# Kernel optimization log

Measured on AMD Instinct MI355X. Metric: run time of the kernel, lower is better.

Reference implementation:

```python
import jax, jax.numpy as jnp
import numpy as np

EPS = 1e-5          # calc_mean_std eps
C = 256             # feature channels
N_PER = 32          # patches per side-group
SIDES = (24, 32, 48)
OUT = 56            # AdaptiveAvgPool2d target


def _pool_matrix(s, o=OUT):
    """Exact torch AdaptiveAvgPool2d as a [o, s] averaging matrix."""
    P = np.zeros((o, s), np.float32)
    for i in range(o):
        start = (i * s) // o
        end = -((-(i + 1) * s) // o)  # ceil((i+1)*s/o)
        P[i, start:end] = 1.0 / (end - start)
    return jnp.asarray(P)

_POOL = {s: _pool_matrix(s) for s in SIDES}


def setup_inputs() -> dict:
    key = jax.random.key(0)
    ks = jax.random.split(key, len(SIDES))
    out = {}
    means, stds = [], []
    for k, s in zip(ks, SIDES):
        raw = jax.random.normal(k, (N_PER, C, s, s), dtype=jnp.float32)
        # calc_mean_std: per (patch, channel) spatial mean / unbiased std
        m = raw.mean(axis=(2, 3), keepdims=True)
        v = raw.var(axis=(2, 3), keepdims=True, ddof=1)
        sd = jnp.sqrt(v + EPS)
        out[f"patches_{s}"] = (raw - m) / sd  # pre-normalized, as in __init__
        means.append(m)
        stds.append(sd)
    out["style_mean"] = jnp.concatenate(means, axis=0)  # [96, C, 1, 1]
    out["style_std"] = jnp.concatenate(stds, axis=0)    # [96, C, 1, 1]
    return out


def _denorm_relu_pool(x, mean, std, P):
    # x: [n, C, s, s]; affine denorm + ReLU + adaptive avg pool to 56x56
    t = jax.nn.relu(x * std + mean)
    y = jnp.einsum('oi,ncij->ncoj', P, t)   # pool rows
    y = jnp.einsum('ncoj,pj->ncop', y, P)   # pool cols
    return y


def reference(patches_24, patches_32, patches_48, style_mean, style_std):
    groups = ((patches_24, 24, 0), (patches_32, 32, N_PER), (patches_48, 48, 2 * N_PER))
    outs = []
    for x, s, lo in groups:
        n = x.shape[0]
        outs.append(_denorm_relu_pool(x, style_mean[lo:lo + n], style_std[lo:lo + n], _POOL[s]))
    return jnp.concatenate(outs, axis=0)  # [96, C, 56, 56]
```

## Files before the change

### kernel.cpp

```cpp
#include <hip/hip_runtime.h>


#define C_CH 256
#define OUTS 56
#define NPER 32

template<int S>
__device__ __forceinline__ void group_body(const float* __restrict__ x,
                                           const float* __restrict__ smean,
                                           const float* __restrict__ sstd,
                                           float* __restrict__ out,
                                           int local_bid, int n_base,
                                           float* __restrict__ lds) {
    const int n_local = local_bid >> 8;
    const int c       = local_bid & 255;
    const int n_glob  = n_base + n_local;
    const float mn = smean[n_glob * C_CH + c];
    const float sd = sstd [n_glob * C_CH + c];

    const float* xin = x + (size_t)(n_local * C_CH + c) * (S * S);
    const int tid = threadIdx.x;

    constexpr int NV = (S * S) / 4;
    const float4* x4 = (const float4*)xin;
    float4* l4 = (float4*)lds;
    for (int idx = tid; idx < NV; idx += 256) {
        float4 v = x4[idx];
        v.x = fmaxf(fmaf(v.x, sd, mn), 0.0f);
        v.y = fmaxf(fmaf(v.y, sd, mn), 0.0f);
        v.z = fmaxf(fmaf(v.z, sd, mn), 0.0f);
        v.w = fmaxf(fmaf(v.w, sd, mn), 0.0f);
        l4[idx] = v;
    }
    __syncthreads();

    float* outp = out + (size_t)(n_glob * C_CH + c) * (OUTS * OUTS);
    float4* out4 = (float4*)outp;

    constexpr int NQ = (OUTS * OUTS) / 4;
    for (int q = tid; q < NQ; q += 256) {
        const int i  = q / (OUTS / 4);
        const int j0 = (q % (OUTS / 4)) * 4;
        const int r0 = (i * S) / OUTS;
        const int r1 = ((i + 1) * S + OUTS - 1) / OUTS;
        const int rc = r1 - r0;

        float o[4];
        #pragma unroll
        for (int k = 0; k < 4; ++k) {
            const int j  = j0 + k;
            const int c0 = (j * S) / OUTS;
            const int c1 = ((j + 1) * S + OUTS - 1) / OUTS;
            const int cc = c1 - c0;
            float acc = lds[r0 * S + c0];
            if (cc == 2) acc += lds[r0 * S + c0 + 1];
            if (rc == 2) {
                acc += lds[(r0 + 1) * S + c0];
                if (cc == 2) acc += lds[(r0 + 1) * S + c0 + 1];
            }
            o[k] = acc * (1.0f / (float)(rc * cc));
        }
        float4 v; v.x = o[0]; v.y = o[1]; v.z = o[2]; v.w = o[3];
        out4[q] = v;
    }
}

__global__ __launch_bounds__(256) void PPIN_DC_20753281974843_kernel(
        const float* __restrict__ p24, const float* __restrict__ p32,
        const float* __restrict__ p48, const float* __restrict__ smean,
        const float* __restrict__ sstd, float* __restrict__ out) {
    __shared__ float lds[48 * 48];
    const int bid   = blockIdx.x;
    const int group = bid >> 13;
    const int local = bid & 8191;
    if (group == 0)      group_body<24>(p24, smean, sstd, out, local, 0,        lds);
    else if (group == 1) group_body<32>(p32, smean, sstd, out, local, NPER,     lds);
    else                 group_body<48>(p48, smean, sstd, out, local, 2 * NPER, lds);
}

extern "C" void kernel_launch(void* const* d_in, const int* in_sizes, int n_in,
                              void* d_out, int out_size, void* d_ws, size_t ws_size,
                              hipStream_t stream) {
    const float* p24   = (const float*)d_in[0];
    const float* p32   = (const float*)d_in[1];
    const float* p48   = (const float*)d_in[2];
    const float* smean = (const float*)d_in[3];
    const float* sstd  = (const float*)d_in[4];
    float* out = (float*)d_out;

    PPIN_DC_20753281974843_kernel<<<dim3(24576), dim3(256), 0, stream>>>(
        p24, p32, p48, smean, sstd, out);
}
```

Measured before the change: 391.4 us.

## Process two channels per block with interleaved LDS and branchless 2x2 pooling

Measured after the change: 401.0 us. 2.4% more time.

```diff
diff --git a/kernel.cpp b/kernel.cpp
--- a/kernel.cpp
+++ b/kernel.cpp
@@ -11,57 +11,71 @@
                                            const float* __restrict__ sstd,
                                            float* __restrict__ out,
                                            int local_bid, int n_base,
-                                           float* __restrict__ lds) {
-    const int n_local = local_bid >> 8;
-    const int c       = local_bid & 255;
+                                           float2* __restrict__ lds2) {
+    const int n_local = local_bid >> 7;
+    const int pair    = local_bid & 127;
+    const int ch      = pair * 2;
     const int n_glob  = n_base + n_local;
-    const float mn = smean[n_glob * C_CH + c];
-    const float sd = sstd [n_glob * C_CH + c];
 
-    const float* xin = x + (size_t)(n_local * C_CH + c) * (S * S);
+    const float2 mn = *(const float2*)(smean + n_glob * C_CH + ch);
+    const float2 sd = *(const float2*)(sstd  + n_glob * C_CH + ch);
+
+    const float* xa = x + (size_t)(n_local * C_CH + ch) * (S * S);
+    const float4* a4 = (const float4*)xa;
+    const float4* b4 = (const float4*)(xa + S * S);
+    float4* l4 = (float4*)lds2;
+
     const int tid = threadIdx.x;
 
     constexpr int NV = (S * S) / 4;
-    const float4* x4 = (const float4*)xin;
-    float4* l4 = (float4*)lds;
     for (int idx = tid; idx < NV; idx += 256) {
-        float4 v = x4[idx];
-        v.x = fmaxf(fmaf(v.x, sd, mn), 0.0f);
-        v.y = fmaxf(fmaf(v.y, sd, mn), 0.0f);
-        v.z = fmaxf(fmaf(v.z, sd, mn), 0.0f);
-        v.w = fmaxf(fmaf(v.w, sd, mn), 0.0f);
-        l4[idx] = v;
+        float4 va = a4[idx];
+        float4 vb = b4[idx];
+        va.x = fmaxf(fmaf(va.x, sd.x, mn.x), 0.0f);
+        va.y = fmaxf(fmaf(va.y, sd.x, mn.x), 0.0f);
+        va.z = fmaxf(fmaf(va.z, sd.x, mn.x), 0.0f);
+        va.w = fmaxf(fmaf(va.w, sd.x, mn.x), 0.0f);
+        vb.x = fmaxf(fmaf(vb.x, sd.y, mn.y), 0.0f);
+        vb.y = fmaxf(fmaf(vb.y, sd.y, mn.y), 0.0f);
+        vb.z = fmaxf(fmaf(vb.z, sd.y, mn.y), 0.0f);
+        vb.w = fmaxf(fmaf(vb.w, sd.y, mn.y), 0.0f);
+        float4 lo; lo.x = va.x; lo.y = vb.x; lo.z = va.y; lo.w = vb.y;
+        float4 hi; hi.x = va.z; hi.y = vb.z; hi.z = va.w; hi.w = vb.w;
+        l4[2 * idx]     = lo;
+        l4[2 * idx + 1] = hi;
     }
     __syncthreads();
 
-    float* outp = out + (size_t)(n_glob * C_CH + c) * (OUTS * OUTS);
-    float4* out4 = (float4*)outp;
+    float* outA = out + (size_t)(n_glob * C_CH + ch) * (OUTS * OUTS);
+    float4* oa4 = (float4*)outA;
+    float4* ob4 = (float4*)(outA + OUTS * OUTS);
 
     constexpr int NQ = (OUTS * OUTS) / 4;
     for (int q = tid; q < NQ; q += 256) {
         const int i  = q / (OUTS / 4);
-        const int j0 = (q % (OUTS / 4)) * 4;
-        const int r0 = (i * S) / OUTS;
-        const int r1 = ((i + 1) * S + OUTS - 1) / OUTS;
-        const int rc = r1 - r0;
+        const int j0 = (q - i * (OUTS / 4)) * 4;
+        const int rA = (i * S) / OUTS;
+        const int rB = ((i + 1) * S - 1) / OUTS;
+        const float2* rowA = lds2 + rA * S;
+        const float2* rowB = lds2 + rB * S;
 
-        float o[4];
+        float oA[4], oB[4];
         #pragma unroll
         for (int k = 0; k < 4; ++k) {
             const int j  = j0 + k;
-            const int c0 = (j * S) / OUTS;
-            const int c1 = ((j + 1) * S + OUTS - 1) / OUTS;
-            const int cc = c1 - c0;
-            float acc = lds[r0 * S + c0];
-            if (cc == 2) acc += lds[r0 * S + c0 + 1];
-            if (rc == 2) {
-                acc += lds[(r0 + 1) * S + c0];
-                if (cc == 2) acc += lds[(r0 + 1) * S + c0 + 1];
-            }
-            o[k] = acc * (1.0f / (float)(rc * cc));
+            const int cA = (j * S) / OUTS;
+            const int cB = ((j + 1) * S - 1) / OUTS;
+            const float2 v0 = rowA[cA];
+            const float2 v1 = rowA[cB];
+            const float2 v2 = rowB[cA];
+            const float2 v3 = rowB[cB];
+            oA[k] = 0.25f * ((v0.x + v1.x) + (v2.x + v3.x));
+            oB[k] = 0.25f * ((v0.y + v1.y) + (v2.y + v3.y));
         }
-        float4 v; v.x = o[0]; v.y = o[1]; v.z = o[2]; v.w = o[3];
-        out4[q] = v;
+        float4 sa; sa.x = oA[0]; sa.y = oA[1]; sa.z = oA[2]; sa.w = oA[3];
+        float4 sb; sb.x = oB[0]; sb.y = oB[1]; sb.z = oB[2]; sb.w = oB[3];
+        oa4[q] = sa;
+        ob4[q] = sb;
     }
 }
 
@@ -69,13 +83,13 @@
         const float* __restrict__ p24, const float* __restrict__ p32,
         const float* __restrict__ p48, const float* __restrict__ smean,
         const float* __restrict__ sstd, float* __restrict__ out) {
-    __shared__ float lds[48 * 48];
+    __shared__ float2 lds2[48 * 48];
     const int bid   = blockIdx.x;
-    const int group = bid >> 13;
-    const int local = bid & 8191;
-    if (group == 0)      group_body<24>(p24, smean, sstd, out, local, 0,        lds);
-    else if (group == 1) group_body<32>(p32, smean, sstd, out, local, NPER,     lds);
-    else                 group_body<48>(p48, smean, sstd, out, local, 2 * NPER, lds);
+    const int group = bid >> 12;
+    const int local = bid & 4095;
+    if (group == 0)      group_body<24>(p24, smean, sstd, out, local, 0,        lds2);
+    else if (group == 1) group_body<32>(p32, smean, sstd, out, local, NPER,     lds2);
+    else                 group_body<48>(p48, smean, sstd, out, local, 2 * NPER, lds2);
 }
 
 extern "C" void kernel_launch(void* const* d_in, const int* in_sizes, int n_in,
@@ -88,6 +102,6 @@
     const float* sstd  = (const float*)d_in[4];
     float* out = (float*)d_out;
 
-    PPIN_DC_20753281974843_kernel<<<dim3(24576), dim3(256), 0, stream>>>(
+    PPIN_DC_20753281974843_kernel<<<dim3(12288), dim3(256), 0, stream>>>(
         p24, p32, p48, smean, sstd, out);
 }
```
